# Performance work log

Hardware: AMD Instinct MI355X
Metric: run time of the kernel (lower is better)

Reference implementation:

```python
import jax, jax.numpy as jnp
import numpy as np
import math

SCALES = [1.0, 0.9, 0.8, 0.7, 0.6]
SOFTMAX_SCALE = 10.0
RES_SCALE = 1.0
ESCAPE_NAN = 1e-4


def _prelu(x, a):
    return jnp.where(x >= 0, x, a * x)


def _conv1x1(x, W, b, a):
    # x: [B,C,H,W], W: [O,C], b: [O], a: [1] (PReLU slope)
    y = jnp.einsum('oc,bchw->bohw', W, x) + b[None, :, None, None]
    return _prelu(y, a[0])


def _cubic_weight(t):
    # Keys cubic kernel, a=-0.75 (matches torch bicubic)
    a = -0.75
    at = jnp.abs(t)
    w1 = ((a + 2.0) * at - (a + 3.0)) * at * at + 1.0
    w2 = (((at - 5.0) * at + 8.0) * at - 4.0) * a
    return jnp.where(at <= 1.0, w1, jnp.where(at < 2.0, w2, 0.0))


def _resize_axis(x, out_size, axis):
    # bicubic, align_corners=True, border-clamped (matches F.interpolate)
    in_size = x.shape[axis]
    x = jnp.moveaxis(x, axis, -1)
    scale = (in_size - 1) / (out_size - 1)
    src = jnp.arange(out_size, dtype=jnp.float32) * jnp.float32(scale)
    i0f = jnp.floor(src)
    frac = src - i0f
    i0 = i0f.astype(jnp.int32)
    idx = jnp.stack([jnp.clip(i0 + d, 0, in_size - 1) for d in (-1, 0, 1, 2)], 0)  # [4,out]
    wts = jnp.stack([_cubic_weight(frac - d) for d in (-1, 0, 1, 2)], 0)            # [4,out]
    g = x[..., idx]                                                                  # [...,4,out]
    y = jnp.einsum('...ko,ko->...o', g, wts)
    return jnp.moveaxis(y, -1, axis)


def _bicubic(x, oh, ow):
    return _resize_axis(_resize_axis(x, oh, 2), ow, 3)


def _extract_patches3(x):
    # 3x3 patches, stride 1, 'same' pad -> [B, H*W, C*9], ordered (C, kh, kw)
    B, C, H, W = x.shape
    xp = jnp.pad(x, ((0, 0), (0, 0), (1, 1), (1, 1)))
    p = jnp.stack([xp[:, :, di:di + H, dj:dj + W]
                   for di in range(3) for dj in range(3)], axis=2)  # [B,C,9,H,W]
    return p.transpose(0, 3, 4, 1, 2).reshape(B, H * W, C * 9)


def _conv_transpose_per_sample(y, w):
    # y: [L,H,W], w: [L,C,3,3]; conv_transpose2d stride=1 pad=1 == conv with flipped, transposed kernel
    wf = jnp.transpose(w[:, :, ::-1, ::-1], (1, 0, 2, 3))  # [C,L,3,3]
    out = jax.lax.conv_general_dilated(
        y[None], wf, window_strides=(1, 1), padding=((1, 1), (1, 1)),
        dimension_numbers=('NCHW', 'OIHW', 'NCHW'))
    return out[0]


def _forward(x, W_mb, b_mb, a_mb, W_m, b_m, a_m, W_a, b_a, a_a):
    B, C, H, W = x.shape
    match_base = _conv1x1(x, W_mb, b_mb, a_mb)      # [B,25,H,W]
    xq = _extract_patches3(match_base)               # [B,HW,225] query patches
    w_list, raw_list = [], []
    for s in SCALES:
        if s == 1.0:
            ref = x
        else:
            ref = _bicubic(x, int(math.floor(H * s)), int(math.floor(W * s)))
        base = _conv1x1(ref, W_a, b_a, a_a)          # [B,C,h,w] assembly (values)
        raw_list.append(_extract_patches3(base).reshape(B, -1, C, 3, 3))
        m = _conv1x1(ref, W_m, b_m, a_m)             # [B,25,h,w] keys
        w_list.append(_extract_patches3(m))          # [B,Li,225]
    wcat = jnp.concatenate(w_list, axis=1)           # [B,L,225]
    rawcat = jnp.concatenate(raw_list, axis=1)       # [B,L,C,3,3]
    norm = jnp.sqrt(jnp.sum(wcat * wcat, axis=-1, keepdims=True))
    wn = wcat / jnp.maximum(norm, ESCAPE_NAN)
    scores = jnp.einsum('blk,bpk->blp', wn, xq) * SOFTMAX_SCALE  # [B,L,HW]
    attn = jax.nn.softmax(scores, axis=1).reshape(B, -1, H, W)    # [B,L,H,W]
    y = jax.vmap(_conv_transpose_per_sample)(attn, rawcat) / 4.0  # [B,C,H,W]
    return y + x * RES_SCALE


def setup_inputs() -> dict:
    key = jax.random.key(0)
    ks = jax.random.split(key, 4)
    B, C, H, W = 2, 50, 48, 48
    Cr = C // 2
    return {
        'x': jax.random.normal(ks[0], (B, C, H, W), jnp.float32),
        'W_mb': jax.random.normal(ks[1], (Cr, C), jnp.float32) * 0.1,
        'b_mb': jnp.zeros((Cr,), jnp.float32),
        'a_mb': jnp.full((1,), 0.25, jnp.float32),
        'W_m': jax.random.normal(ks[2], (Cr, C), jnp.float32) * 0.1,
        'b_m': jnp.zeros((Cr,), jnp.float32),
        'a_m': jnp.full((1,), 0.25, jnp.float32),
        'W_a': jax.random.normal(ks[3], (C, C), jnp.float32) * 0.1,
        'b_a': jnp.zeros((C,), jnp.float32),
        'a_a': jnp.full((1,), 0.25, jnp.float32),
    }


def reference(x, W_mb, b_mb, a_mb, W_m, b_m, a_m, W_a, b_a, a_a):
    return _forward(x, W_mb, b_mb, a_mb, W_m, b_m, a_m, W_a, b_a, a_a)
```

## Files before the change

### kernel.cpp

```cpp
#include <hip/hip_runtime.h>
#include <math.h>

#define NB 2
#define NC 50
#define NCR 25
#define H0 48
#define W0 48
#define HW0 2304
#define LTOT 7470
#define LP 7552
#define K225 225
#define KP 256
#define CD 450
#define CDP 512
#define NSPLIT 8
#define KCHUNK 960

typedef _Float16 f16x8 __attribute__((ext_vector_type(8)));
typedef float f32x4 __attribute__((ext_vector_type(4)));

#define GLOAD_LDS16(gp, lp) __builtin_amdgcn_global_load_lds( \
    (const __attribute__((address_space(1))) void*)(gp),      \
    (__attribute__((address_space(3))) void*)(lp), 16, 0, 0)

__device__ __forceinline__ void decode_pix(int pix, int& s, int& off, int& d) {
  if (pix < 2304)      { s = 0; off = 0;    d = 48; }
  else if (pix < 4153) { s = 1; off = 2304; d = 43; }
  else if (pix < 5597) { s = 2; off = 4153; d = 38; }
  else if (pix < 6686) { s = 3; off = 5597; d = 33; }
  else                 { s = 4; off = 6686; d = 28; }
}

__device__ __forceinline__ float cubw(float t) {
  const float a = -0.75f;
  float at = fabsf(t);
  float w1 = ((a + 2.f) * at - (a + 3.f)) * at * at + 1.f;
  float w2 = (((at - 5.f) * at + 8.f) * at - 4.f) * a;
  return at <= 1.f ? w1 : (at < 2.f ? w2 : 0.f);
}

__global__ void k_conv1x1(const float* __restrict__ in, const float* __restrict__ Wt,
                          const float* __restrict__ bias, const float* __restrict__ slope,
                          float* __restrict__ out, int Cin, int O, int P) {
  int t = blockIdx.x * blockDim.x + threadIdx.x;
  int total = NB * O * P;
  if (t >= total) return;
  int pix = t % P;
  int o = (t / P) % O;
  int b = t / (P * O);
  float acc = bias[o];
  const float* ip = in + (size_t)b * Cin * P + pix;
  const float* wr = Wt + o * Cin;
  for (int c = 0; c < Cin; ++c) acc = fmaf(wr[c], ip[(size_t)c * P], acc);
  float a = slope[0];
  out[t] = acc >= 0.f ? acc : a * acc;
}

__global__ void k_conv_bm(const float* __restrict__ refs,
                          const float* __restrict__ Wa, const float* __restrict__ ba,
                          const float* __restrict__ aa,
                          const float* __restrict__ Wm, const float* __restrict__ bm,
                          const float* __restrict__ am,
                          float* __restrict__ base, float* __restrict__ m) {
  int t = blockIdx.x * blockDim.x + threadIdx.x;
  int total = NB * (NC + NCR) * LTOT;
  if (t >= total) return;
  int pix = t % LTOT;
  int o = (t / LTOT) % (NC + NCR);
  int b = t / (LTOT * (NC + NCR));
  const float* ip = refs + (size_t)b * NC * LTOT + pix;
  const float* wr;
  float acc, a;
  float* dst;
  if (o < NC) {
    wr = Wa + o * NC; acc = ba[o]; a = aa[0];
    dst = base + ((size_t)b * NC + o) * LTOT + pix;
  } else {
    int o2 = o - NC;
    wr = Wm + o2 * NC; acc = bm[o2]; a = am[0];
    dst = m + ((size_t)b * NCR + o2) * LTOT + pix;
  }
  for (int c = 0; c < NC; ++c) acc = fmaf(wr[c], ip[(size_t)c * LTOT], acc);
  *dst = acc >= 0.f ? acc : a * acc;
}

__global__ void k_build_refs(const float* __restrict__ x, float* __restrict__ refs) {
  int t = blockIdx.x * blockDim.x + threadIdx.x;
  int total = NB * NC * LTOT;
  if (t >= total) return;
  int pix = t % LTOT;
  int c = (t / LTOT) % NC;
  int b = t / (LTOT * NC);
  int s, off, d;
  decode_pix(pix, s, off, d);
  float v;
  const float* xb = x + ((size_t)b * NC + c) * HW0;
  if (s == 0) {
    v = xb[pix];
  } else {
    int rem = pix - off;
    int oy = rem / d, ox = rem % d;
    float scale = 47.f / (float)(d - 1);
    float sy = oy * scale, sx = ox * scale;
    float fy0 = floorf(sy), fx0 = floorf(sx);
    int iy = (int)fy0, ix = (int)fx0;
    float fy = sy - fy0, fx = sx - fx0;
    float wy[4], wx[4];
#pragma unroll
    for (int dd = 0; dd < 4; ++dd) {
      wy[dd] = cubw(fy - (float)(dd - 1));
      wx[dd] = cubw(fx - (float)(dd - 1));
    }
    float acc = 0.f;
#pragma unroll
    for (int p = 0; p < 4; ++p) {
      int yy = min(max(iy + p - 1, 0), 47);
      float rowacc = 0.f;
#pragma unroll
      for (int q = 0; q < 4; ++q) {
        int xx = min(max(ix + q - 1, 0), 47);
        rowacc = fmaf(wx[q], xb[yy * 48 + xx], rowacc);
      }
      acc = fmaf(wy[p], rowacc, acc);
    }
    v = acc;
  }
  refs[t] = v;
}

__global__ void k_build_xq(const float* __restrict__ mb, _Float16* __restrict__ xq) {
  int bp = blockIdx.x;
  int b = bp / HW0, p = bp % HW0;
  int i = p / W0, j = p % W0;
  int k = threadIdx.x;
  float v = 0.f;
  if (k < K225) {
    int c = k / 9, r = k % 9, di = r / 3, dj = r % 3;
    int yy = i + di - 1, xx = j + dj - 1;
    if (yy >= 0 && yy < H0 && xx >= 0 && xx < W0)
      v = mb[((size_t)b * NCR + c) * HW0 + yy * W0 + xx];
  }
  xq[(size_t)bp * KP + k] = (_Float16)v;
}

__global__ void k_build_wn(const float* __restrict__ m, _Float16* __restrict__ wn) {
  __shared__ float red[256];
  int bl = blockIdx.x;
  int b = bl / LP, l = bl % LP;
  int k = threadIdx.x;
  if (l >= LTOT) {
    wn[(size_t)bl * KP + k] = (_Float16)0.f;
    return;
  }
  int s, off, d;
  decode_pix(l, s, off, d);
  int rem = l - off;
  int y = rem / d, x = rem % d;
  float v = 0.f;
  if (k < K225) {
    int c = k / 9, r = k % 9, di = r / 3, dj = r % 3;
    int yy = y + di - 1, xx = x + dj - 1;
    if (yy >= 0 && yy < d && xx >= 0 && xx < d)
      v = m[((size_t)b * NCR + c) * LTOT + off + yy * d + xx];
  }
  red[k] = v * v;
  __syncthreads();
  for (int st = 128; st > 0; st >>= 1) {
    if (k < st) red[k] += red[k + st];
    __syncthreads();
  }
  float norm = sqrtf(red[0]);
  float sc = 10.f / fmaxf(norm, 1e-4f);
  wn[(size_t)bl * KP + k] = (_Float16)(v * sc);
}

__global__ void k_build_brawT(const float* __restrict__ base, _Float16* __restrict__ BT) {
  int t = blockIdx.x * blockDim.x + threadIdx.x;
  int total = NB * CDP * LP;
  if (t >= total) return;
  int l = t % LP;
  int cd = (t / LP) % CDP;
  int b = t / (LP * CDP);
  float v = 0.f;
  if (cd < CD && l < LTOT) {
    int s, off, d;
    decode_pix(l, s, off, d);
    int rem = l - off;
    int y = rem / d, x = rem % d;
    int c = cd / 9, r = cd % 9, di = r / 3, dj = r % 3;
    int yy = y + di - 1, xx = x + dj - 1;
    if (yy >= 0 && yy < d && xx >= 0 && xx < d)
      v = 0.25f * base[((size_t)b * NC + c) * LTOT + off + yy * d + xx];
  }
  BT[t] = (_Float16)v;
}

__global__ __launch_bounds__(256) void k_gemm_nt_f16(
    const _Float16* __restrict__ A, const _Float16* __restrict__ Bm,
    _Float16* __restrict__ Cm, int K, int lda, int ldb, int ldc,
    long long sA, long long sB, long long sC) {
  __shared__ _Float16 As[128 * 32];
  __shared__ _Float16 Bs[128 * 32];
  const _Float16* Ab = A + blockIdx.z * sA;
  const _Float16* Bb = Bm + blockIdx.z * sB;
  _Float16* Cb = Cm + blockIdx.z * sC;
  int m0 = blockIdx.y * 128, n0 = blockIdx.x * 128;
  int t = threadIdx.x;
  int lane = t & 63, wid = t >> 6;
  int wr = wid >> 1, wc = wid & 1;
  f32x4 acc[4][4] = {};
  for (int k0 = 0; k0 < K; k0 += 32) {
#pragma unroll
    for (int i = 0; i < 2; ++i) {
      int e = i * 256 + t;
      int r = e >> 2, c = e & 3;
      GLOAD_LDS16(Ab + (size_t)(m0 + r) * lda + k0 + c * 8, As + (size_t)e * 8);
      GLOAD_LDS16(Bb + (size_t)(n0 + r) * ldb + k0 + c * 8, Bs + (size_t)e * 8);
    }
    __syncthreads();
    int rla = (wr * 64 + (lane & 15)) * 32 + (lane >> 4) * 8;
    int rlb = (wc * 64 + (lane & 15)) * 32 + (lane >> 4) * 8;
    f16x8 af[4], bf[4];
#pragma unroll
    for (int mi = 0; mi < 4; ++mi) af[mi] = *(const f16x8*)&As[rla + mi * 16 * 32];
#pragma unroll
    for (int ni = 0; ni < 4; ++ni) bf[ni] = *(const f16x8*)&Bs[rlb + ni * 16 * 32];
#pragma unroll
    for (int mi = 0; mi < 4; ++mi)
#pragma unroll
      for (int ni = 0; ni < 4; ++ni)
        acc[mi][ni] = __builtin_amdgcn_mfma_f32_16x16x32_f16(af[mi], bf[ni], acc[mi][ni], 0, 0, 0);
    __syncthreads();
  }
  int col0 = lane & 15;
  int row0 = (lane >> 4) * 4;
#pragma unroll
  for (int mi = 0; mi < 4; ++mi) {
#pragma unroll
    for (int ni = 0; ni < 4; ++ni) {
      int n = n0 + wc * 64 + ni * 16 + col0;
#pragma unroll
      for (int r = 0; r < 4; ++r) {
        int mrow = m0 + wr * 64 + mi * 16 + row0 + r;
        Cb[(size_t)mrow * ldc + n] = (_Float16)acc[mi][ni][r];
      }
    }
  }
}

__global__ __launch_bounds__(512) void k_gemm2(
    const _Float16* __restrict__ A, const _Float16* __restrict__ Bm,
    _Float16* __restrict__ Cm, int lda, int ldb, int ldc,
    long long sA, long long sB, long long sC) {
  __shared__ _Float16 As[128 * 32];
  __shared__ _Float16 Bs[256 * 32];
  int z = blockIdx.z;
  int b = z / NSPLIT, s = z % NSPLIT;
  int kbeg = s * KCHUNK;
  int klen = min(KCHUNK, LP - kbeg);
  const _Float16* Ab = A + b * sA + (size_t)kbeg;
  const _Float16* Bb = Bm + b * sB + (size_t)kbeg;
  _Float16* Cb = Cm + z * sC;
  int m0 = blockIdx.y * 128, n0 = blockIdx.x * 256;
  int t = threadIdx.x;
  int lane = t & 63, wid = t >> 6;
  int wr = wid >> 2, wc = wid & 3;
  f32x4 acc[4][4] = {};
  for (int k0 = 0; k0 < klen; k0 += 32) {
    {
      int e = t;
      int r = e >> 2, c = e & 3;
      GLOAD_LDS16(Ab + (size_t)(m0 + r) * lda + k0 + c * 8, As + (size_t)e * 8);
    }
#pragma unroll
    for (int i = 0; i < 2; ++i) {
      int e = i * 512 + t;
      int r = e >> 2, c = e & 3;
      GLOAD_LDS16(Bb + (size_t)(n0 + r) * ldb + k0 + c * 8, Bs + (size_t)e * 8);
    }
    __syncthreads();
    int rla = (wr * 64 + (lane & 15)) * 32 + (lane >> 4) * 8;
    int rlb = (wc * 64 + (lane & 15)) * 32 + (lane >> 4) * 8;
    f16x8 af[4], bf[4];
#pragma unroll
    for (int mi = 0; mi < 4; ++mi) af[mi] = *(const f16x8*)&As[rla + mi * 16 * 32];
#pragma unroll
    for (int ni = 0; ni < 4; ++ni) bf[ni] = *(const f16x8*)&Bs[rlb + ni * 16 * 32];
#pragma unroll
    for (int mi = 0; mi < 4; ++mi)
#pragma unroll
      for (int ni = 0; ni < 4; ++ni)
        acc[mi][ni] = __builtin_amdgcn_mfma_f32_16x16x32_f16(af[mi], bf[ni], acc[mi][ni], 0, 0, 0);
    __syncthreads();
  }
  int col0 = lane & 15;
  int row0 = (lane >> 4) * 4;
#pragma unroll
  for (int mi = 0; mi < 4; ++mi) {
#pragma unroll
    for (int ni = 0; ni < 4; ++ni) {
      int n = n0 + wc * 64 + ni * 16 + col0;
#pragma unroll
      for (int r = 0; r < 4; ++r) {
        int mrow = m0 + wr * 64 + mi * 16 + row0 + r;
        Cb[(size_t)mrow * ldc + n] = (_Float16)acc[mi][ni][r];
      }
    }
  }
}

__global__ void k_softmax16(_Float16* __restrict__ S) {
  __shared__ float buf[LTOT];
  __shared__ float red[256];
  size_t row = blockIdx.x;
  _Float16* r = S + row * LP;
  f16x8* r8 = (f16x8*)r;
  int tid = threadIdx.x;
  float mx = -1e30f;
  for (int ch = tid; ch < LP / 8; ch += 256) {
    f16x8 v = r8[ch];
    int base = ch * 8;
#pragma unroll
    for (int j = 0; j < 8; ++j) {
      int l = base + j;
      if (l < LTOT) {
        float f = (float)v[j];
        buf[l] = f;
        mx = fmaxf(mx, f);
      }
    }
  }
  red[tid] = mx;
  __syncthreads();
  for (int st = 128; st > 0; st >>= 1) {
    if (tid < st) red[tid] = fmaxf(red[tid], red[tid + st]);
    __syncthreads();
  }
  mx = red[0];
  __syncthreads();
  float sm = 0.f;
  for (int i = tid; i < LTOT; i += 256) {
    float e = __expf(buf[i] - mx);
    buf[i] = e;
    sm += e;
  }
  red[tid] = sm;
  __syncthreads();
  for (int st = 128; st > 0; st >>= 1) {
    if (tid < st) red[tid] += red[tid + st];
    __syncthreads();
  }
  float inv = 1.f / red[0];
  __syncthreads();
  for (int ch = tid; ch < LP / 8; ch += 256) {
    int base = ch * 8;
    f16x8 o;
#pragma unroll
    for (int j = 0; j < 8; ++j) {
      int l = base + j;
      o[j] = (l < LTOT) ? (_Float16)(buf[l] * inv) : (_Float16)0.f;
    }
    r8[ch] = o;
  }
}

__global__ void k_reduceG(const _Float16* __restrict__ Gp, float* __restrict__ G,
                          int pc, int p0) {
  int t = blockIdx.x * blockDim.x + threadIdx.x;
  int total = NB * pc * CD;
  if (t >= total) return;
  int cd = t % CD;
  int p = (t / CD) % pc;
  int b = t / (CD * pc);
  float acc = 0.f;
#pragma unroll
  for (int s = 0; s < NSPLIT; ++s)
    acc += (float)Gp[(((size_t)(b * NSPLIT + s) * pc) + p) * CDP + cd];
  G[((size_t)b * HW0 + p0 + p) * CD + cd] = acc;
}

__global__ void k_final(const float* __restrict__ G, const float* __restrict__ x,
                        float* __restrict__ out) {
  int t = blockIdx.x * blockDim.x + threadIdx.x;
  int total = NB * NC * HW0;
  if (t >= total) return;
  int p = t % HW0;
  int c = (t / HW0) % NC;
  int b = t / (HW0 * NC);
  int i = p / W0, j = p % W0;
  float sum = 0.f;
#pragma unroll
  for (int kh = 0; kh < 3; ++kh) {
    int pi = i - kh + 1;
    if (pi < 0 || pi >= H0) continue;
#pragma unroll
    for (int kw = 0; kw < 3; ++kw) {
      int pj = j - kw + 1;
      if (pj < 0 || pj >= W0) continue;
      sum += G[((size_t)b * HW0 + pi * W0 + pj) * CD + c * 9 + kh * 3 + kw];
    }
  }
  out[t] = sum + x[t];
}

static inline size_t rup(size_t x) { return (x + 255) & ~(size_t)255; }

extern "C" void kernel_launch(void* const* d_in, const int* in_sizes, int n_in,
                              void* d_out, int out_size, void* d_ws, size_t ws_size,
                              hipStream_t stream) {
  const float* x   = (const float*)d_in[0];
  const float* Wmb = (const float*)d_in[1];
  const float* bmb = (const float*)d_in[2];
  const float* amb = (const float*)d_in[3];
  const float* Wm  = (const float*)d_in[4];
  const float* bm  = (const float*)d_in[5];
  const float* am  = (const float*)d_in[6];
  const float* Wa  = (const float*)d_in[7];
  const float* ba  = (const float*)d_in[8];
  const float* aa  = (const float*)d_in[9];
  float* out = (float*)d_out;
  char* ws = (char*)d_ws;

  size_t off = 0;
  float* mb    = (float*)(ws + off); off = rup(off + sizeof(float) * NB * NCR * HW0);
  float* refs  = (float*)(ws + off); off = rup(off + sizeof(float) * NB * NC * LTOT);
  float* base  = (float*)(ws + off); off = rup(off + sizeof(float) * NB * NC * LTOT);
  float* m     = (float*)(ws + off); off = rup(off + sizeof(float) * NB * NCR * LTOT);
  _Float16* xq16 = (_Float16*)(ws + off); off = rup(off + sizeof(_Float16) * NB * HW0 * KP);
  _Float16* wn16 = (_Float16*)(ws + off); off = rup(off + sizeof(_Float16) * (size_t)NB * LP * KP);
  _Float16* bt16 = (_Float16*)(ws + off); off = rup(off + sizeof(_Float16) * (size_t)NB * CDP * LP);
  float* G     = (float*)(ws + off); off = rup(off + sizeof(float) * NB * HW0 * CD);

  int pc = HW0;
  {
    size_t avail = (ws_size > off) ? ws_size - off - 1024 : 0;
    size_t per = (size_t)NB * (LP * 2 + NSPLIT * CDP * 2);
    while (pc > 128 && (size_t)pc * per > avail) {
      if (pc == HW0) pc = 1152;
      else if (pc == 1152) pc = 768;
      else if (pc == 768) pc = 384;
      else pc = 128;
    }
  }
  _Float16* scbuf16 = (_Float16*)(ws + off); off = rup(off + sizeof(_Float16) * (size_t)NB * pc * LP);
  _Float16* Gp = (_Float16*)(ws + off);

  const int th = 256;
  k_conv1x1<<<(NB * NCR * HW0 + th - 1) / th, th, 0, stream>>>(x, Wmb, bmb, amb, mb, NC, NCR, HW0);
  k_build_refs<<<(NB * NC * LTOT + th - 1) / th, th, 0, stream>>>(x, refs);
  k_conv_bm<<<(NB * (NC + NCR) * LTOT + th - 1) / th, th, 0, stream>>>(
      refs, Wa, ba, aa, Wm, bm, am, base, m);
  k_build_xq<<<NB * HW0, 256, 0, stream>>>(mb, xq16);
  k_build_wn<<<NB * LP, 256, 0, stream>>>(m, wn16);
  k_build_brawT<<<(NB * CDP * LP + th - 1) / th, th, 0, stream>>>(base, bt16);

  for (int p0 = 0; p0 < HW0; p0 += pc) {
    dim3 g1(LP / 128, pc / 128, NB);
    k_gemm_nt_f16<<<g1, 256, 0, stream>>>(
        xq16 + (size_t)p0 * KP, wn16, scbuf16,
        KP, KP, KP, LP,
        (long long)HW0 * KP, (long long)LP * KP, (long long)pc * LP);
    k_softmax16<<<NB * pc, 256, 0, stream>>>(scbuf16);
    dim3 g2(CDP / 256, pc / 128, NB * NSPLIT);
    k_gemm2<<<g2, 512, 0, stream>>>(
        scbuf16, bt16, Gp,
        LP, LP, CDP,
        (long long)pc * LP, (long long)CDP * LP, (long long)pc * CDP);
    k_reduceG<<<(NB * pc * CD + th - 1) / th, th, 0, stream>>>(Gp, G, pc, p0);
  }
  k_final<<<(NB * NC * HW0 + th - 1) / th, th, 0, stream>>>(G, x, out);
}
```

Measured before the change: 314.6 us.

## Double-buffer LDS tiles in both f16 MFMA GEMM kernels

Both GEMM kernels now keep two LDS buffers for the A and B tiles. The global-to-LDS loads for the next K step are issued before the MFMA work on the current tile, so load latency can overlap with compute, and one barrier per iteration is removed. In exchange, LDS use per block doubles, which may reduce occupancy. The barrier must also wait for the async global_load_lds operations to finish before the next iteration reads that buffer.

```diff
diff --git a/kernel.cpp b/kernel.cpp
--- a/kernel.cpp
+++ b/kernel.cpp
@@ -199,8 +199,8 @@
     const _Float16* __restrict__ A, const _Float16* __restrict__ Bm,
     _Float16* __restrict__ Cm, int K, int lda, int ldb, int ldc,
     long long sA, long long sB, long long sC) {
-  __shared__ _Float16 As[128 * 32];
-  __shared__ _Float16 Bs[128 * 32];
+  __shared__ _Float16 As[2][128 * 32];
+  __shared__ _Float16 Bs[2][128 * 32];
   const _Float16* Ab = A + blockIdx.z * sA;
   const _Float16* Bb = Bm + blockIdx.z * sB;
   _Float16* Cb = Cm + blockIdx.z * sC;
@@ -208,29 +208,40 @@
   int t = threadIdx.x;
   int lane = t & 63, wid = t >> 6;
   int wr = wid >> 1, wc = wid & 1;
+  int r = t >> 2, c4 = t & 3;
   f32x4 acc[4][4] = {};
+
+#define G1_STAGE(buf, k0)                                                        \
+  {                                                                              \
+    GLOAD_LDS16(Ab + (size_t)(m0 + r) * lda + (k0) + c4 * 8,                     \
+                As[buf] + (size_t)t * 8);                                        \
+    GLOAD_LDS16(Ab + (size_t)(m0 + 64 + r) * lda + (k0) + c4 * 8,                \
+                As[buf] + (size_t)(256 + t) * 8);                                \
+    GLOAD_LDS16(Bb + (size_t)(n0 + r) * ldb + (k0) + c4 * 8,                     \
+                Bs[buf] + (size_t)t * 8);                                        \
+    GLOAD_LDS16(Bb + (size_t)(n0 + 64 + r) * ldb + (k0) + c4 * 8,                \
+                Bs[buf] + (size_t)(256 + t) * 8);                                \
+  }
+
+  G1_STAGE(0, 0);
+  __syncthreads();
+  int cur = 0;
   for (int k0 = 0; k0 < K; k0 += 32) {
-#pragma unroll
-    for (int i = 0; i < 2; ++i) {
-      int e = i * 256 + t;
-      int r = e >> 2, c = e & 3;
-      GLOAD_LDS16(Ab + (size_t)(m0 + r) * lda + k0 + c * 8, As + (size_t)e * 8);
-      GLOAD_LDS16(Bb + (size_t)(n0 + r) * ldb + k0 + c * 8, Bs + (size_t)e * 8);
-    }
-    __syncthreads();
+    if (k0 + 32 < K) G1_STAGE(cur ^ 1, k0 + 32);
     int rla = (wr * 64 + (lane & 15)) * 32 + (lane >> 4) * 8;
     int rlb = (wc * 64 + (lane & 15)) * 32 + (lane >> 4) * 8;
     f16x8 af[4], bf[4];
 #pragma unroll
-    for (int mi = 0; mi < 4; ++mi) af[mi] = *(const f16x8*)&As[rla + mi * 16 * 32];
-#pragma unroll
-    for (int ni = 0; ni < 4; ++ni) bf[ni] = *(const f16x8*)&Bs[rlb + ni * 16 * 32];
+    for (int mi = 0; mi < 4; ++mi) af[mi] = *(const f16x8*)&As[cur][rla + mi * 16 * 32];
+#pragma unroll
+    for (int ni = 0; ni < 4; ++ni) bf[ni] = *(const f16x8*)&Bs[cur][rlb + ni * 16 * 32];
 #pragma unroll
     for (int mi = 0; mi < 4; ++mi)
 #pragma unroll
       for (int ni = 0; ni < 4; ++ni)
         acc[mi][ni] = __builtin_amdgcn_mfma_f32_16x16x32_f16(af[mi], bf[ni], acc[mi][ni], 0, 0, 0);
     __syncthreads();
+    cur ^= 1;
   }
   int col0 = lane & 15;
   int row0 = (lane >> 4) * 4;
@@ -240,9 +251,9 @@
     for (int ni = 0; ni < 4; ++ni) {
       int n = n0 + wc * 64 + ni * 16 + col0;
 #pragma unroll
-      for (int r = 0; r < 4; ++r) {
-        int mrow = m0 + wr * 64 + mi * 16 + row0 + r;
-        Cb[(size_t)mrow * ldc + n] = (_Float16)acc[mi][ni][r];
+      for (int rr = 0; rr < 4; ++rr) {
+        int mrow = m0 + wr * 64 + mi * 16 + row0 + rr;
+        Cb[(size_t)mrow * ldc + n] = (_Float16)acc[mi][ni][rr];
       }
     }
   }
@@ -252,8 +263,8 @@
     const _Float16* __restrict__ A, const _Float16* __restrict__ Bm,
     _Float16* __restrict__ Cm, int lda, int ldb, int ldc,
     long long sA, long long sB, long long sC) {
-  __shared__ _Float16 As[128 * 32];
-  __shared__ _Float16 Bs[256 * 32];
+  __shared__ _Float16 As[2][128 * 32];
+  __shared__ _Float16 Bs[2][256 * 32];
   int z = blockIdx.z;
   int b = z / NSPLIT, s = z % NSPLIT;
   int kbeg = s * KCHUNK;
@@ -265,33 +276,38 @@
   int t = threadIdx.x;
   int lane = t & 63, wid = t >> 6;
   int wr = wid >> 2, wc = wid & 3;
+  int r = t >> 2, c4 = t & 3;
+
+#define G2_STAGE(buf, k0)                                                        \
+  {                                                                              \
+    GLOAD_LDS16(Ab + (size_t)(m0 + r) * lda + (k0) + c4 * 8,                     \
+                As[buf] + (size_t)t * 8);                                        \
+    GLOAD_LDS16(Bb + (size_t)(n0 + r) * ldb + (k0) + c4 * 8,                     \
+                Bs[buf] + (size_t)t * 8);                                        \
+    GLOAD_LDS16(Bb + (size_t)(n0 + 128 + r) * ldb + (k0) + c4 * 8,               \
+                Bs[buf] + (size_t)(512 + t) * 8);                                \
+  }
+
   f32x4 acc[4][4] = {};
+  G2_STAGE(0, 0);
+  __syncthreads();
+  int cur = 0;
   for (int k0 = 0; k0 < klen; k0 += 32) {
-    {
-      int e = t;
-      int r = e >> 2, c = e & 3;
-      GLOAD_LDS16(Ab + (size_t)(m0 + r) * lda + k0 + c * 8, As + (size_t)e * 8);
-    }
-#pragma unroll
-    for (int i = 0; i < 2; ++i) {
-      int e = i * 512 + t;
-      int r = e >> 2, c = e & 3;
-      GLOAD_LDS16(Bb + (size_t)(n0 + r) * ldb + k0 + c * 8, Bs + (size_t)e * 8);
-    }
-    __syncthreads();
+    if (k0 + 32 < klen) G2_STAGE(cur ^ 1, k0 + 32);
     int rla = (wr * 64 + (lane & 15)) * 32 + (lane >> 4) * 8;
     int rlb = (wc * 64 + (lane & 15)) * 32 + (lane >> 4) * 8;
     f16x8 af[4], bf[4];
 #pragma unroll
-    for (int mi = 0; mi < 4; ++mi) af[mi] = *(const f16x8*)&As[rla + mi * 16 * 32];
-#pragma unroll
-    for (int ni = 0; ni < 4; ++ni) bf[ni] = *(const f16x8*)&Bs[rlb + ni * 16 * 32];
+    for (int mi = 0; mi < 4; ++mi) af[mi] = *(const f16x8*)&As[cur][rla + mi * 16 * 32];
+#pragma unroll
+    for (int ni = 0; ni < 4; ++ni) bf[ni] = *(const f16x8*)&Bs[cur][rlb + ni * 16 * 32];
 #pragma unroll
     for (int mi = 0; mi < 4; ++mi)
 #pragma unroll
       for (int ni = 0; ni < 4; ++ni)
         acc[mi][ni] = __builtin_amdgcn_mfma_f32_16x16x32_f16(af[mi], bf[ni], acc[mi][ni], 0, 0, 0);
     __syncthreads();
+    cur ^= 1;
   }
   int col0 = lane & 15;
   int row0 = (lane >> 4) * 4;
@@ -301,9 +317,9 @@
     for (int ni = 0; ni < 4; ++ni) {
       int n = n0 + wc * 64 + ni * 16 + col0;
 #pragma unroll
-      for (int r = 0; r < 4; ++r) {
-        int mrow = m0 + wr * 64 + mi * 16 + row0 + r;
-        Cb[(size_t)mrow * ldc + n] = (_Float16)acc[mi][ni][r];
+      for (int rr = 0; rr < 4; ++rr) {
+        int mrow = m0 + wr * 64 + mi * 16 + row0 + rr;
+        Cb[(size_t)mrow * ldc + n] = (_Float16)acc[mi][ni][rr];
       }
     }
   }
```

Measured after the change: 315.0 us. No clear change (+0.1%).
